# Kernel tuning notes

Hardware: AMD Instinct MI355X
Metric: run time of the kernel (lower is better)

The kernel has to match this reference:

```python
import jax, jax.numpy as jnp
import numpy as np

TAU = 2.0
THRESHOLD = 1.0


def setup_inputs() -> dict:
    key = jax.random.key(0)
    k_x, k_w, k_b = jax.random.split(key, 3)
    B, T, IN, OUT = 64, 512, 1024, 1024
    x = jax.random.normal(k_x, (B, T, IN), dtype=jnp.float32)
    # nn.Linear default init: U(-1/sqrt(in), 1/sqrt(in))
    bound = 1.0 / np.sqrt(IN)
    W = jax.random.uniform(k_w, (OUT, IN), dtype=jnp.float32, minval=-bound, maxval=bound)
    b = jax.random.uniform(k_b, (OUT,), dtype=jnp.float32, minval=-bound, maxval=bound)
    return {"x": x, "W": W, "b": b}


def reference(x, W, b):
    # Precompute the time-independent linear projection: [B, T, OUT]
    proj = jnp.einsum('bti,oi->bto', x, W) + b
    B, T, OUT = proj.shape
    mem0 = jnp.zeros((B, OUT), dtype=proj.dtype)

    def step(mem, inp_t):
        mem = mem + (inp_t - mem) / TAU
        spk = (mem >= THRESHOLD).astype(mem.dtype)
        mem = mem * (1.0 - spk)
        return mem, spk

    # scan over time: carry mem, keep only the last spk
    mem_final, spks = jax.lax.scan(step, mem0, jnp.swapaxes(proj, 0, 1))
    spk_final = spks[-1]
    return mem_final, spk_final
```

## Files before the change

kernel.cpp:

```cpp
#include <hip/hip_runtime.h>
#include <cstdint>
#include <cstddef>

typedef _Float16 f16;
typedef __attribute__((ext_vector_type(8))) _Float16 half8;
typedef __attribute__((ext_vector_type(4))) _Float16 half4;
typedef __attribute__((ext_vector_type(4))) float f32x4;

#define IN_DIM   1024
#define OUT_DIM  1024
#define T_STEPS  512
#define B_TOTAL  64

#define GLDS16(g, l)                                                            \
    __builtin_amdgcn_global_load_lds(                                           \
        (const __attribute__((address_space(1))) void*)(g),                     \
        (__attribute__((address_space(3))) void*)(l), 16, 0, 0)

__global__ __launch_bounds__(256)
void split_f32_f16(const float* __restrict__ in,
                   f16* __restrict__ hi, f16* __restrict__ lo, int n4)
{
    const int i = blockIdx.x * 256 + threadIdx.x;
    if (i >= n4) return;
    const float4 v = reinterpret_cast<const float4*>(in)[i];
    const float xs[4] = { v.x, v.y, v.z, v.w };
    half4 h, l;
#pragma unroll
    for (int j = 0; j < 4; ++j) {
        const f16 hh = (f16)xs[j];
        h[j] = hh;
        l[j] = (f16)((xs[j] - (float)hh) * 2048.0f);
    }
    reinterpret_cast<half4*>(hi)[i] = h;
    reinterpret_cast<half4*>(lo)[i] = l;
}

__global__ __launch_bounds__(256, 2)
void gemm_f16x3(const f16* __restrict__ Ahg, const f16* __restrict__ Alg,
                const f16* __restrict__ Bhg, const f16* __restrict__ Blg,
                const float* __restrict__ bias, float* __restrict__ C)
{
    __shared__ f16 Ah[128][32];
    __shared__ f16 Al[128][32];
    __shared__ f16 Bh[128][32];
    __shared__ f16 Bl[128][32];

    const int tid  = threadIdx.x;
    const int lane = tid & 63;
    const int wave = tid >> 6;
    const int wr   = wave >> 1;
    const int wc   = wave & 1;
    const int lr   = lane & 15;
    const int lq   = lane >> 4;
    const int bn   = blockIdx.x;
    const int bm   = blockIdx.y;

    f32x4 accH[4][4], accL[4][4];
#pragma unroll
    for (int i = 0; i < 4; ++i)
#pragma unroll
        for (int j = 0; j < 4; ++j) {
            accH[i][j] = (f32x4){0.f, 0.f, 0.f, 0.f};
            accL[i][j] = (f32x4){0.f, 0.f, 0.f, 0.f};
        }

    const int r0  = tid >> 2;
    const int r1  = (tid + 256) >> 2;
    const int cb  = (tid & 3) * 16;
    const char* ApH = (const char*)(Ahg + (size_t)(bm * 128) * IN_DIM);
    const char* ApL = (const char*)(Alg + (size_t)(bm * 128) * IN_DIM);
    const char* BpH = (const char*)(Bhg + (size_t)(bn * 128) * IN_DIM);
    const char* BpL = (const char*)(Blg + (size_t)(bn * 128) * IN_DIM);
    char* lAh = (char*)&Ah[0][0] + tid * 16;
    char* lAl = (char*)&Al[0][0] + tid * 16;
    char* lBh = (char*)&Bh[0][0] + tid * 16;
    char* lBl = (char*)&Bl[0][0] + tid * 16;

    for (int k0 = 0; k0 < IN_DIM; k0 += 32) {
        __syncthreads();
        const size_t o0 = (size_t)r0 * (IN_DIM * 2) + k0 * 2 + cb;
        const size_t o1 = (size_t)r1 * (IN_DIM * 2) + k0 * 2 + cb;
        GLDS16(ApH + o0, lAh);
        GLDS16(ApH + o1, lAh + 4096);
        GLDS16(ApL + o0, lAl);
        GLDS16(ApL + o1, lAl + 4096);
        GLDS16(BpH + o0, lBh);
        GLDS16(BpH + o1, lBh + 4096);
        GLDS16(BpL + o0, lBl);
        GLDS16(BpL + o1, lBl + 4096);
        __syncthreads();

        half8 a_h[4], a_l[4];
#pragma unroll
        for (int i = 0; i < 4; ++i) {
            const int row = wr * 64 + i * 16 + lr;
            a_h[i] = *reinterpret_cast<const half8*>(&Ah[row][lq * 8]);
            a_l[i] = *reinterpret_cast<const half8*>(&Al[row][lq * 8]);
        }
#pragma unroll
        for (int j = 0; j < 4; ++j) {
            const int col = wc * 64 + j * 16 + lr;
            const half8 b_h = *reinterpret_cast<const half8*>(&Bh[col][lq * 8]);
            const half8 b_l = *reinterpret_cast<const half8*>(&Bl[col][lq * 8]);
#pragma unroll
            for (int i = 0; i < 4; ++i)
                accH[i][j] = __builtin_amdgcn_mfma_f32_16x16x32_f16(a_h[i], b_h, accH[i][j], 0, 0, 0);
#pragma unroll
            for (int i = 0; i < 4; ++i)
                accL[i][j] = __builtin_amdgcn_mfma_f32_16x16x32_f16(a_l[i], b_h, accL[i][j], 0, 0, 0);
#pragma unroll
            for (int i = 0; i < 4; ++i)
                accL[i][j] = __builtin_amdgcn_mfma_f32_16x16x32_f16(a_h[i], b_l, accL[i][j], 0, 0, 0);
        }
    }

    float bv[4];
#pragma unroll
    for (int j = 0; j < 4; ++j)
        bv[j] = bias[bn * 128 + wc * 64 + j * 16 + lr];
#pragma unroll
    for (int i = 0; i < 4; ++i) {
#pragma unroll
        for (int r = 0; r < 4; ++r) {
            const int row = bm * 128 + wr * 64 + i * 16 + lq * 4 + r;
            float* Cr = C + (size_t)row * OUT_DIM;
#pragma unroll
            for (int j = 0; j < 4; ++j) {
                const int col = bn * 128 + wc * 64 + j * 16 + lr;
                Cr[col] = accH[i][j][r] + 0.00048828125f * accL[i][j][r] + bv[j];
            }
        }
    }
}

__global__ __launch_bounds__(256)
void lif_scan(const float* __restrict__ proj,
              float* __restrict__ out_mem, float* __restrict__ out_spk,
              int b_off)
{
    const int tid = blockIdx.x * 256 + threadIdx.x;
    const int b = tid >> 10;
    const int o = tid & 1023;
    const float* p = proj + (size_t)b * (T_STEPS * OUT_DIM) + o;

    float mem = 0.f, spk = 0.f;
    for (int t0 = 0; t0 < T_STEPS; t0 += 16) {
        float buf[16];
#pragma unroll
        for (int u = 0; u < 16; ++u)
            buf[u] = p[(size_t)(t0 + u) * OUT_DIM];
#pragma unroll
        for (int u = 0; u < 16; ++u) {
            mem = mem + (buf[u] - mem) * 0.5f;
            const bool fire = (mem >= 1.0f);
            spk = fire ? 1.0f : 0.0f;
            mem = fire ? 0.0f : mem;
        }
    }
    const size_t oi = (size_t)(b_off + b) * OUT_DIM + o;
    out_mem[oi] = mem;
    out_spk[oi] = spk;
}

extern "C" void kernel_launch(void* const* d_in, const int* in_sizes, int n_in,
                              void* d_out, int out_size, void* d_ws, size_t ws_size,
                              hipStream_t stream)
{
    const float* x    = (const float*)d_in[0];
    const float* W    = (const float*)d_in[1];
    const float* bias = (const float*)d_in[2];

    float* out_mem = (float*)d_out;
    float* out_spk = out_mem + (size_t)B_TOTAL * OUT_DIM;

    const size_t MB = 1u << 20;
    char* ws = (char*)d_ws;
    f16* whi = (f16*)ws;
    f16* wlo = (f16*)(ws + 2 * MB);
    char* base = ws + 4 * MB;

    int Bc = (int)((ws_size - 4 * MB) / (4 * MB));
    if (Bc > B_TOTAL) Bc = B_TOTAL;
    if (Bc < 1) Bc = 1;

    f16*   xhi  = (f16*)base;
    f16*   xlo  = (f16*)(base + (size_t)Bc * MB);
    float* proj = (float*)(base + 2 * (size_t)Bc * MB);

    split_f32_f16<<<1024, 256, 0, stream>>>(W, whi, wlo, 262144);

    for (int b0 = 0; b0 < B_TOTAL; b0 += Bc) {
        const int bc = (B_TOTAL - b0 < Bc) ? (B_TOTAL - b0) : Bc;
        split_f32_f16<<<bc * 512, 256, 0, stream>>>(
            x + (size_t)b0 * T_STEPS * IN_DIM, xhi, xlo, bc * 131072);
        gemm_f16x3<<<dim3(OUT_DIM / 128, bc * 4), 256, 0, stream>>>(
            xhi, xlo, whi, wlo, bias, proj);
        lif_scan<<<bc * 4, 256, 0, stream>>>(proj, out_mem, out_spk, b0);
    }
}
```

Measured before the change: 468.9 us.

## Fold f16x3 split into K=3072 GEMM with 256x256 pipelined tiles

```diff
diff --git a/kernel.cpp b/kernel.cpp
--- a/kernel.cpp
+++ b/kernel.cpp
@@ -11,127 +11,182 @@
 #define OUT_DIM  1024
 #define T_STEPS  512
 #define B_TOTAL  64
+#define K3       3072
+#define NTILES   48
+
+#define RT2048   45.254833995939045f
+#define IRT2048  0.0220970869120796f
 
 #define GLDS16(g, l)                                                            \
     __builtin_amdgcn_global_load_lds(                                           \
         (const __attribute__((address_space(1))) void*)(g),                     \
         (__attribute__((address_space(3))) void*)(l), 16, 0, 0)
 
+#define MEMFENCE asm volatile("" ::: "memory")
+#define SBAR     do { MEMFENCE; __builtin_amdgcn_s_barrier(); MEMFENCE; } while (0)
+#define VMCNT(n) asm volatile("s_waitcnt vmcnt(" #n ")" ::: "memory")
+
 __global__ __launch_bounds__(256)
-void split_f32_f16(const float* __restrict__ in,
-                   f16* __restrict__ hi, f16* __restrict__ lo, int n4)
-{
-    const int i = blockIdx.x * 256 + threadIdx.x;
-    if (i >= n4) return;
-    const float4 v = reinterpret_cast<const float4*>(in)[i];
+void split3(const float* __restrict__ in, f16* __restrict__ out, int mode)
+{
+    const int i4 = blockIdx.x * 256 + threadIdx.x;
+    const int m  = i4 >> 8;
+    const int kc = (i4 & 255) * 4;
+    const float4 v = reinterpret_cast<const float4*>(in)[i4];
     const float xs[4] = { v.x, v.y, v.z, v.w };
-    half4 h, l;
-#pragma unroll
-    for (int j = 0; j < 4; ++j) {
-        const f16 hh = (f16)xs[j];
-        h[j] = hh;
-        l[j] = (f16)((xs[j] - (float)hh) * 2048.0f);
-    }
-    reinterpret_cast<half4*>(hi)[i] = h;
-    reinterpret_cast<half4*>(lo)[i] = l;
-}
-
-__global__ __launch_bounds__(256, 2)
-void gemm_f16x3(const f16* __restrict__ Ahg, const f16* __restrict__ Alg,
-                const f16* __restrict__ Bhg, const f16* __restrict__ Blg,
-                const float* __restrict__ bias, float* __restrict__ C)
-{
-    __shared__ f16 Ah[128][32];
-    __shared__ f16 Al[128][32];
-    __shared__ f16 Bh[128][32];
-    __shared__ f16 Bl[128][32];
+    half4 h, lo, ch;
+#pragma unroll
+    for (int e = 0; e < 4; ++e) {
+        const f16 hh = (f16)xs[e];
+        h[e]  = hh;
+        lo[e] = (f16)((xs[e] - (float)hh) * RT2048 * 2048.0f * (1.0f / 2048.0f) * RT2048);
+        lo[e] = (f16)((xs[e] - (float)hh) * RT2048);
+        ch[e] = (f16)((float)hh * IRT2048);
+    }
+    f16* row = out + (size_t)m * K3;
+    *reinterpret_cast<half4*>(row + kc)                    = h;
+    *reinterpret_cast<half4*>(row + 1024 + kc)             = mode ? ch : lo;
+    *reinterpret_cast<half4*>(row + 2048 + kc)             = mode ? lo : ch;
+}
+
+__global__ __launch_bounds__(512, 2)
+void gemm8(const f16* __restrict__ Ap, const f16* __restrict__ Bp,
+           const float* __restrict__ bias, float* __restrict__ C, int cpx)
+{
+    extern __shared__ char smem[];
 
     const int tid  = threadIdx.x;
     const int lane = tid & 63;
     const int wave = tid >> 6;
-    const int wr   = wave >> 1;
-    const int wc   = wave & 1;
+    const int wm   = wave >> 2;
+    const int wn   = wave & 3;
     const int lr   = lane & 15;
-    const int lq   = lane >> 4;
-    const int bn   = blockIdx.x;
-    const int bm   = blockIdx.y;
-
-    f32x4 accH[4][4], accL[4][4];
-#pragma unroll
-    for (int i = 0; i < 4; ++i)
-#pragma unroll
-        for (int j = 0; j < 4; ++j) {
-            accH[i][j] = (f32x4){0.f, 0.f, 0.f, 0.f};
-            accL[i][j] = (f32x4){0.f, 0.f, 0.f, 0.f};
-        }
-
-    const int r0  = tid >> 2;
-    const int r1  = (tid + 256) >> 2;
-    const int cb  = (tid & 3) * 16;
-    const char* ApH = (const char*)(Ahg + (size_t)(bm * 128) * IN_DIM);
-    const char* ApL = (const char*)(Alg + (size_t)(bm * 128) * IN_DIM);
-    const char* BpH = (const char*)(Bhg + (size_t)(bn * 128) * IN_DIM);
-    const char* BpL = (const char*)(Blg + (size_t)(bn * 128) * IN_DIM);
-    char* lAh = (char*)&Ah[0][0] + tid * 16;
-    char* lAl = (char*)&Al[0][0] + tid * 16;
-    char* lBh = (char*)&Bh[0][0] + tid * 16;
-    char* lBl = (char*)&Bl[0][0] + tid * 16;
-
-    for (int k0 = 0; k0 < IN_DIM; k0 += 32) {
-        __syncthreads();
-        const size_t o0 = (size_t)r0 * (IN_DIM * 2) + k0 * 2 + cb;
-        const size_t o1 = (size_t)r1 * (IN_DIM * 2) + k0 * 2 + cb;
-        GLDS16(ApH + o0, lAh);
-        GLDS16(ApH + o1, lAh + 4096);
-        GLDS16(ApL + o0, lAl);
-        GLDS16(ApL + o1, lAl + 4096);
-        GLDS16(BpH + o0, lBh);
-        GLDS16(BpH + o1, lBh + 4096);
-        GLDS16(BpL + o0, lBl);
-        GLDS16(BpL + o1, lBl + 4096);
-        __syncthreads();
-
-        half8 a_h[4], a_l[4];
+    const int lq16 = (lane >> 4) * 16;
+    const int rsw  = (lr & 1) << 6;
+
+    const int bid = blockIdx.x;
+    const int swz = (bid & 7) * cpx + (bid >> 3);
+    const int mt  = swz >> 2;
+    const int nt  = swz & 3;
+
+    const f16* Ag = Ap + (size_t)(mt * 256) * K3;
+    const f16* Bg = Bp + (size_t)(nt * 256) * K3;
+
+#define STAGE(bufb, isB, j, kt) do {                                            \
+        const int Drel_ = (j) * 8192 + tid * 16;                                \
+        const int rw_   = Drel_ >> 7;                                           \
+        const int kb_   = (Drel_ & 127) ^ ((rw_ & 1) << 6);                     \
+        const char* g_  = (const char*)((isB) ? Bg : Ag)                        \
+                          + (size_t)rw_ * (K3 * 2) + (kt) * 128 + kb_;          \
+        GLDS16(g_, smem + (bufb) * 65536 + (isB) * 32768 + Drel_);              \
+    } while (0)
+
+#define LDS_A(bufb, row, ks) \
+    (*(const half8*)(smem + (bufb) * 65536 + (row) * 128 + (((ks) * 64 + lq16) ^ rsw)))
+#define LDS_B(bufb, row, ks) \
+    (*(const half8*)(smem + (bufb) * 65536 + 32768 + (row) * 128 + (((ks) * 64 + lq16) ^ rsw)))
+
+    f32x4 acc[8][4];
+#pragma unroll
+    for (int i = 0; i < 8; ++i)
+#pragma unroll
+        for (int j = 0; j < 4; ++j) acc[i][j] = (f32x4){0.f, 0.f, 0.f, 0.f};
+
+    STAGE(0, 0, 0, 0); STAGE(0, 0, 1, 0); STAGE(0, 0, 2, 0); STAGE(0, 0, 3, 0);
+    STAGE(0, 1, 0, 0); STAGE(0, 1, 1, 0); STAGE(0, 1, 2, 0); STAGE(0, 1, 3, 0);
+    STAGE(1, 1, 0, 1); STAGE(1, 1, 1, 1); STAGE(1, 1, 2, 1); STAGE(1, 1, 3, 1);
+    VMCNT(4);
+    SBAR;
+
+    half8 a_[4][2], bf[4][2];
+
+    for (int t = 0; t < NTILES; ++t) {
+        const int cur = t & 1;
+        const int nxt = cur ^ 1;
+
 #pragma unroll
         for (int i = 0; i < 4; ++i) {
-            const int row = wr * 64 + i * 16 + lr;
-            a_h[i] = *reinterpret_cast<const half8*>(&Ah[row][lq * 8]);
-            a_l[i] = *reinterpret_cast<const half8*>(&Al[row][lq * 8]);
-        }
-#pragma unroll
-        for (int j = 0; j < 4; ++j) {
-            const int col = wc * 64 + j * 16 + lr;
-            const half8 b_h = *reinterpret_cast<const half8*>(&Bh[col][lq * 8]);
-            const half8 b_l = *reinterpret_cast<const half8*>(&Bl[col][lq * 8]);
-#pragma unroll
-            for (int i = 0; i < 4; ++i)
-                accH[i][j] = __builtin_amdgcn_mfma_f32_16x16x32_f16(a_h[i], b_h, accH[i][j], 0, 0, 0);
-#pragma unroll
-            for (int i = 0; i < 4; ++i)
-                accL[i][j] = __builtin_amdgcn_mfma_f32_16x16x32_f16(a_l[i], b_h, accL[i][j], 0, 0, 0);
-#pragma unroll
-            for (int i = 0; i < 4; ++i)
-                accL[i][j] = __builtin_amdgcn_mfma_f32_16x16x32_f16(a_h[i], b_l, accL[i][j], 0, 0, 0);
-        }
+            const int row = wm * 128 + i * 16 + lr;
+            a_[i][0] = LDS_A(cur, row, 0);
+            a_[i][1] = LDS_A(cur, row, 1);
+        }
+#pragma unroll
+        for (int j = 0; j < 4; ++j)
+            bf[j][0] = LDS_B(cur, wn * 64 + j * 16 + lr, 0);
+        if (t + 1 < NTILES) { STAGE(nxt, 0, 0, t + 1); STAGE(nxt, 0, 1, t + 1); }
+        SBAR;
+        __builtin_amdgcn_s_setprio(1);
+#pragma unroll
+        for (int j = 0; j < 4; ++j)
+#pragma unroll
+            for (int i = 0; i < 4; ++i)
+                acc[i][j] = __builtin_amdgcn_mfma_f32_16x16x32_f16(a_[i][0], bf[j][0], acc[i][j], 0, 0, 0);
+        __builtin_amdgcn_s_setprio(0);
+        SBAR;
+
+#pragma unroll
+        for (int j = 0; j < 4; ++j)
+            bf[j][1] = LDS_B(cur, wn * 64 + j * 16 + lr, 1);
+        if (t + 1 < NTILES) { STAGE(nxt, 0, 2, t + 1); STAGE(nxt, 0, 3, t + 1); }
+        SBAR;
+        __builtin_amdgcn_s_setprio(1);
+#pragma unroll
+        for (int j = 0; j < 4; ++j)
+#pragma unroll
+            for (int i = 0; i < 4; ++i)
+                acc[i][j] = __builtin_amdgcn_mfma_f32_16x16x32_f16(a_[i][1], bf[j][1], acc[i][j], 0, 0, 0);
+        __builtin_amdgcn_s_setprio(0);
+        SBAR;
+
+#pragma unroll
+        for (int i = 0; i < 4; ++i) {
+            const int row = wm * 128 + 64 + i * 16 + lr;
+            a_[i][0] = LDS_A(cur, row, 0);
+            a_[i][1] = LDS_A(cur, row, 1);
+        }
+        if (t + 2 < NTILES) { STAGE(cur, 1, 0, t + 2); STAGE(cur, 1, 1, t + 2); }
+        SBAR;
+        __builtin_amdgcn_s_setprio(1);
+#pragma unroll
+        for (int j = 0; j < 4; ++j)
+#pragma unroll
+            for (int i = 0; i < 4; ++i)
+                acc[4 + i][j] = __builtin_amdgcn_mfma_f32_16x16x32_f16(a_[i][0], bf[j][0], acc[4 + i][j], 0, 0, 0);
+        __builtin_amdgcn_s_setprio(0);
+        SBAR;
+
+        if (t + 2 < NTILES) { STAGE(cur, 1, 2, t + 2); STAGE(cur, 1, 3, t + 2); }
+        if (t < NTILES - 2) { VMCNT(4); } else { VMCNT(0); }
+        SBAR;
+        __builtin_amdgcn_s_setprio(1);
+#pragma unroll
+        for (int j = 0; j < 4; ++j)
+#pragma unroll
+            for (int i = 0; i < 4; ++i)
+                acc[4 + i][j] = __builtin_amdgcn_mfma_f32_16x16x32_f16(a_[i][1], bf[j][1], acc[4 + i][j], 0, 0, 0);
+        __builtin_amdgcn_s_setprio(0);
+        SBAR;
     }
 
     float bv[4];
 #pragma unroll
     for (int j = 0; j < 4; ++j)
-        bv[j] = bias[bn * 128 + wc * 64 + j * 16 + lr];
-#pragma unroll
-    for (int i = 0; i < 4; ++i) {
+        bv[j] = bias[nt * 256 + wn * 64 + j * 16 + lr];
+    const int lq4 = (lane >> 4) * 4;
+#pragma unroll
+    for (int i = 0; i < 8; ++i) {
 #pragma unroll
         for (int r = 0; r < 4; ++r) {
-            const int row = bm * 128 + wr * 64 + i * 16 + lq * 4 + r;
-            float* Cr = C + (size_t)row * OUT_DIM;
-#pragma unroll
-            for (int j = 0; j < 4; ++j) {
-                const int col = bn * 128 + wc * 64 + j * 16 + lr;
-                Cr[col] = accH[i][j][r] + 0.00048828125f * accL[i][j][r] + bv[j];
-            }
-        }
-    }
+            const int row = mt * 256 + wm * 128 + i * 16 + lq4 + r;
+            float* Cr = C + (size_t)row * OUT_DIM + nt * 256 + wn * 64;
+#pragma unroll
+            for (int j = 0; j < 4; ++j)
+                Cr[j * 16 + lr] = acc[i][j][r] + bv[j];
+        }
+    }
+#undef STAGE
+#undef LDS_A
+#undef LDS_B
 }
 
 __global__ __launch_bounds__(256)
@@ -139,28 +194,46 @@
               float* __restrict__ out_mem, float* __restrict__ out_spk,
               int b_off)
 {
-    const int tid = blockIdx.x * 256 + threadIdx.x;
-    const int b = tid >> 10;
-    const int o = tid & 1023;
-    const float* p = proj + (size_t)b * (T_STEPS * OUT_DIM) + o;
+    __shared__ float sbuf[2][32][256];
+
+    const int tid = threadIdx.x;
+    const int blk = blockIdx.x;
+    const int b   = blk >> 2;
+    const int o0  = (blk & 3) * 256;
+    const float* pb = proj + (size_t)b * (T_STEPS * OUT_DIM);
+
+#define SCAN_STAGE(bufb, s) do {                                                \
+        _Pragma("unroll")                                                       \
+        for (int u = 0; u < 8; ++u) {                                           \
+            const int tt = u * 4 + (tid >> 6);                                  \
+            const int oc = (tid * 4) & 255;                                     \
+            const float* g_ = pb + (size_t)((s) * 32 + tt) * OUT_DIM + o0 + oc; \
+            GLDS16(g_, (char*)&sbuf[bufb][0][0] + u * 4096 + tid * 16);         \
+        }                                                                       \
+    } while (0)
+
+    SCAN_STAGE(0, 0);
 
     float mem = 0.f, spk = 0.f;
-    for (int t0 = 0; t0 < T_STEPS; t0 += 16) {
-        float buf[16];
-#pragma unroll
-        for (int u = 0; u < 16; ++u)
-            buf[u] = p[(size_t)(t0 + u) * OUT_DIM];
-#pragma unroll
-        for (int u = 0; u < 16; ++u) {
-            mem = mem + (buf[u] - mem) * 0.5f;
+    for (int s = 0; s < 16; ++s) {
+        const int cur = s & 1;
+        if (s + 1 < 16) { SCAN_STAGE(cur ^ 1, s + 1); VMCNT(8); }
+        else            { VMCNT(0); }
+        SBAR;
+#pragma unroll
+        for (int u = 0; u < 32; ++u) {
+            const float in = sbuf[cur][u][tid];
+            mem = mem + (in - mem) * 0.5f;
             const bool fire = (mem >= 1.0f);
             spk = fire ? 1.0f : 0.0f;
             mem = fire ? 0.0f : mem;
         }
-    }
-    const size_t oi = (size_t)(b_off + b) * OUT_DIM + o;
+        SBAR;
+    }
+    const size_t oi = (size_t)(b_off + b) * OUT_DIM + o0 + tid;
     out_mem[oi] = mem;
     out_spk[oi] = spk;
+#undef SCAN_STAGE
 }
 
 extern "C" void kernel_launch(void* const* d_in, const int* in_sizes, int n_in,
@@ -176,26 +249,24 @@
 
     const size_t MB = 1u << 20;
     char* ws = (char*)d_ws;
-    f16* whi = (f16*)ws;
-    f16* wlo = (f16*)(ws + 2 * MB);
-    char* base = ws + 4 * MB;
-
-    int Bc = (int)((ws_size - 4 * MB) / (4 * MB));
+    f16* Bp = (f16*)ws;
+    char* base = ws + 6 * MB;
+
+    int Bc = (int)((ws_size - 6 * MB) / (5 * MB));
     if (Bc > B_TOTAL) Bc = B_TOTAL;
     if (Bc < 1) Bc = 1;
 
-    f16*   xhi  = (f16*)base;
-    f16*   xlo  = (f16*)(base + (size_t)Bc * MB);
-    float* proj = (float*)(base + 2 * (size_t)Bc * MB);
-
-    split_f32_f16<<<1024, 256, 0, stream>>>(W, whi, wlo, 262144);
+    f16*   Apx  = (f16*)base;
+    float* proj = (float*)(base + (size_t)Bc * 3 * MB);
+
+    split3<<<1024, 256, 0, stream>>>(W, Bp, 1);
 
     for (int b0 = 0; b0 < B_TOTAL; b0 += Bc) {
         const int bc = (B_TOTAL - b0 < Bc) ? (B_TOTAL - b0) : Bc;
-        split_f32_f16<<<bc * 512, 256, 0, stream>>>(
-            x + (size_t)b0 * T_STEPS * IN_DIM, xhi, xlo, bc * 131072);
-        gemm_f16x3<<<dim3(OUT_DIM / 128, bc * 4), 256, 0, stream>>>(
-            xhi, xlo, whi, wlo, bias, proj);
+        split3<<<bc * 512, 256, 0, stream>>>(
+            x + (size_t)b0 * T_STEPS * IN_DIM, Apx, 0);
+        const int nwg = bc * 8;
+        gemm8<<<nwg, 512, 131072, stream>>>(Apx, Bp, bias, proj, nwg / 8);
         lif_scan<<<bc * 4, 256, 0, stream>>>(proj, out_mem, out_spk, b0);
     }
 }
```

Measured after the change: 467.5 us. About the same (-0.3%).
